# Kernel tuning notes

Hardware: AMD Instinct MI355X
Metric: run time of the kernel (lower is better)

The kernel has to match this reference:

```python
import jax, jax.numpy as jnp
import numpy as np

B, N_LINKS, N_JOINTS, C_L, C_J = 4096, 33, 32, 64, 128

def setup_inputs() -> dict:
    key = jax.random.key(0)
    k1, k2, k3, k4 = jax.random.split(key, 4)
    link_feats = jax.random.normal(k1, (B, N_LINKS, C_L, 16), dtype=jnp.float32)
    joint_feats = jax.random.normal(k2, (B, N_JOINTS, C_J), dtype=jnp.float32)
    # Stacked per-joint Linear weights: [J, C_L*16, C_J], bias [J, C_J]
    fan_in = C_L * 16
    W = jax.random.normal(k3, (N_JOINTS, fan_in, C_J), dtype=jnp.float32) / np.sqrt(fan_in).astype(np.float32)
    b = jax.random.normal(k4, (N_JOINTS, C_J), dtype=jnp.float32) * 0.01
    child_idx = jnp.arange(1, N_JOINTS + 1, dtype=jnp.int64)  # child link of joint j is link j+1
    return {"link_feats": link_feats, "joint_feats": joint_feats, "W": W, "b": b, "child_idx": child_idx}

def reference(link_feats, joint_feats, W, b, child_idx):
    # Gather child-link features per joint: [B, J, C_L, 16] -> flatten to [B, J, C_L*16]
    Bsz = link_feats.shape[0]
    J = child_idx.shape[0]
    x = link_feats[:, child_idx].reshape(Bsz, J, -1)
    # Grouped GEMM over joints (replaces Python loop of tiny Linears), + bias + residual
    return jnp.einsum('bji,jio->bjo', x, W) + b[None, :, :] + joint_feats
```

## Files before the change

### kernel.cpp

```cpp
#include <hip/hip_runtime.h>
#include <hip/hip_bf16.h>

typedef __attribute__((ext_vector_type(8))) short bf16x8;
typedef __attribute__((ext_vector_type(4))) float f32x4;

#define NB    4096
#define NLINK 33
#define NJ    32
#define KTOT  1024
#define CJ    128
#define BM    128
#define BK    64
#define NT    (KTOT / BK)

__device__ short g_Wf[NJ * KTOT * CJ];

static __device__ __forceinline__ short f2bf(float f) {
    unsigned u = __builtin_bit_cast(unsigned, f);
    unsigned r = u + 0x7FFFu + ((u >> 16) & 1u);
    return (short)(r >> 16);
}

__global__ __launch_bounds__(256) void conv_w(const float* __restrict__ W) {
    const int gid = blockIdx.x * 256 + threadIdx.x;
    const int q  = gid & 3;
    const int c  = (gid >> 2) & 127;
    const int kt = (gid >> 9) & 31;
    const int j  = gid >> 14;
    const float* src = W + ((size_t)j * KTOT + kt * 32 + q * 8) * CJ + c;
    bf16x8 v;
    #pragma unroll
    for (int e = 0; e < 8; ++e) v[e] = f2bf(src[(size_t)e * CJ]);
    reinterpret_cast<bf16x8*>(g_Wf)[gid] = v;
}

__global__ __launch_bounds__(512, 4) void joint_gemm(
    const float* __restrict__ link,
    const float* __restrict__ jf,
    const float* __restrict__ bias,
    const int*   __restrict__ child,
    float* __restrict__ out)
{
    __shared__ short lA[2][BM * BK];

    const int tid  = threadIdx.x;
    const int lane = tid & 63;
    const int wave = tid >> 6;
    const int wr   = wave >> 1;
    const int wc   = wave & 1;
    const int q    = lane >> 4;
    const int r    = lane & 15;
    const int xr   = r & 7;

    const int bx = blockIdx.x;
    const int j  = bx & 31;
    const int mt = bx >> 5;
    const int rowbase = mt * BM;
    const int cidx = child[j];

    const int srow   = tid >> 2;
    const int squart = tid & 3;
    const float* abase = link + ((size_t)(rowbase + srow) * NLINK + cidx) * KTOT + squart * 16;
    const int xw = srow & 7;
    const int p0 = (squart * 2) ^ xw;
    const int p1 = p0 ^ 1;

    const bf16x8* wb = reinterpret_cast<const bf16x8*>(g_Wf);
    const size_t bbase = ((size_t)j * 32 * 128 + wc * 64 + r) * 4 + q;

    f32x4  acc[2][4] = {};
    float4 fa4[4];
    bf16x8 Breg[2][4];

    auto loadA = [&](int t) {
        const float4* p = reinterpret_cast<const float4*>(abase + (size_t)t * BK);
        fa4[0] = p[0]; fa4[1] = p[1]; fa4[2] = p[2]; fa4[3] = p[3];
    };
    auto stageA = [&](int b) {
        const float* f = reinterpret_cast<const float*>(fa4);
        bf16x8 v0, v1;
        #pragma unroll
        for (int e = 0; e < 8; ++e) { v0[e] = f2bf(f[e]); v1[e] = f2bf(f[8 + e]); }
        bf16x8* Lw = reinterpret_cast<bf16x8*>(lA[b]) + srow * 8;
        Lw[p0] = v0;
        Lw[p1] = v1;
    };
    auto loadB = [&](int t) {
        #pragma unroll
        for (int kk = 0; kk < 2; ++kk)
            #pragma unroll
            for (int ni = 0; ni < 4; ++ni)
                Breg[kk][ni] = wb[bbase + (size_t)(t * 2 + kk) * 512 + ni * 64];
    };

    loadA(0);
    loadB(0);
    stageA(0);
    loadA(1);
    __syncthreads();

    int cur = 0;
    for (int t = 0; t < NT; ++t) {
        if (t + 1 < NT) stageA(cur ^ 1);
        if (t + 2 < NT) loadA(t + 2);

        const bf16x8* Lr = reinterpret_cast<const bf16x8*>(lA[cur]);
        #pragma unroll
        for (int kk = 0; kk < 2; ++kk) {
            bf16x8 af[2];
            #pragma unroll
            for (int mi = 0; mi < 2; ++mi) {
                const int R = wr * 32 + mi * 16 + r;
                af[mi] = Lr[R * 8 + (((kk << 2) | q) ^ xr)];
            }
            #pragma unroll
            for (int mi = 0; mi < 2; ++mi)
                #pragma unroll
                for (int ni = 0; ni < 4; ++ni)
                    acc[mi][ni] = __builtin_amdgcn_mfma_f32_16x16x32_bf16(
                        af[mi], Breg[kk][ni], acc[mi][ni], 0, 0, 0);
        }

        if (t + 1 < NT) loadB(t + 1);
        __syncthreads();
        cur ^= 1;
    }

    float bv[4];
    #pragma unroll
    for (int ni = 0; ni < 4; ++ni) bv[ni] = bias[j * CJ + wc * 64 + ni * 16 + r];

    #pragma unroll
    for (int mi = 0; mi < 2; ++mi) {
        #pragma unroll
        for (int rr = 0; rr < 4; ++rr) {
            const int bg = rowbase + wr * 32 + mi * 16 + q * 4 + rr;
            const size_t ob = ((size_t)bg * NJ + j) * CJ;
            #pragma unroll
            for (int ni = 0; ni < 4; ++ni) {
                const int o = wc * 64 + ni * 16 + r;
                out[ob + o] = acc[mi][ni][rr] + bv[ni] + jf[ob + o];
            }
        }
    }
}

extern "C" void kernel_launch(void* const* d_in, const int* in_sizes, int n_in,
                              void* d_out, int out_size, void* d_ws, size_t ws_size,
                              hipStream_t stream) {
    (void)in_sizes; (void)n_in; (void)out_size; (void)d_ws; (void)ws_size;
    const float* link  = (const float*)d_in[0];
    const float* jfeat = (const float*)d_in[1];
    const float* W     = (const float*)d_in[2];
    const float* bias  = (const float*)d_in[3];
    const int*   child = (const int*)d_in[4];
    float* out = (float*)d_out;

    conv_w<<<dim3((NJ * KTOT * CJ / 8) / 256), dim3(256), 0, stream>>>(W);
    joint_gemm<<<dim3(NJ * (NB / BM)), dim3(512), 0, stream>>>(link, jfeat, bias, child, out);
}
```

Baseline: 182.3 us.

## Drop LDS staging and feed MFMA A-fragments directly from registers

Removes the shared-memory A tile and its per-step __syncthreads. Each wave now loads its own 32 fp32 rows straight into registers in MFMA fragment layout and converts them to bf16 there. Each block shrinks to 4 waves, and each wave covers all 128 output columns, with a two-stage register double buffer for both A and B. The aim is to cut LDS traffic and barrier stalls in a memory-bound gather-GEMM. The cost is much higher register pressure (launch bounds of 256 threads, 2 blocks) and lower occupancy, which may leave too little memory latency hidden.

```diff
diff --git a/kernel.cpp b/kernel.cpp
--- a/kernel.cpp
+++ b/kernel.cpp
@@ -1,5 +1,4 @@
 #include <hip/hip_runtime.h>
-#include <hip/hip_bf16.h>
 
 typedef __attribute__((ext_vector_type(8))) short bf16x8;
 typedef __attribute__((ext_vector_type(4))) float f32x4;
@@ -9,9 +8,7 @@
 #define NJ    32
 #define KTOT  1024
 #define CJ    128
-#define BM    128
-#define BK    64
-#define NT    (KTOT / BK)
+#define NSTEP 32
 
 __device__ short g_Wf[NJ * KTOT * CJ];
 
@@ -34,111 +31,92 @@
     reinterpret_cast<bf16x8*>(g_Wf)[gid] = v;
 }
 
-__global__ __launch_bounds__(512, 4) void joint_gemm(
+__global__ __launch_bounds__(256, 2) void joint_gemm(
     const float* __restrict__ link,
     const float* __restrict__ jf,
     const float* __restrict__ bias,
     const int*   __restrict__ child,
     float* __restrict__ out)
 {
-    __shared__ short lA[2][BM * BK];
-
     const int tid  = threadIdx.x;
     const int lane = tid & 63;
     const int wave = tid >> 6;
-    const int wr   = wave >> 1;
-    const int wc   = wave & 1;
     const int q    = lane >> 4;
     const int r    = lane & 15;
-    const int xr   = r & 7;
 
     const int bx = blockIdx.x;
     const int j  = bx & 31;
     const int mt = bx >> 5;
-    const int rowbase = mt * BM;
+    const int row0 = mt * 128 + wave * 32;
     const int cidx = child[j];
 
-    const int srow   = tid >> 2;
-    const int squart = tid & 3;
-    const float* abase = link + ((size_t)(rowbase + srow) * NLINK + cidx) * KTOT + squart * 16;
-    const int xw = srow & 7;
-    const int p0 = (squart * 2) ^ xw;
-    const int p1 = p0 ^ 1;
+    const float* a0 = link + ((size_t)(row0 + r) * NLINK + cidx) * KTOT + q * 8;
+    const float* a1 = a0 + (size_t)16 * NLINK * KTOT;
 
     const bf16x8* wb = reinterpret_cast<const bf16x8*>(g_Wf);
-    const size_t bbase = ((size_t)j * 32 * 128 + wc * 64 + r) * 4 + q;
+    const size_t bb = ((size_t)j * 32 * 128 + r) * 4 + q;
 
-    f32x4  acc[2][4] = {};
-    float4 fa4[4];
-    bf16x8 Breg[2][4];
+    f32x4 acc[2][8] = {};
 
-    auto loadA = [&](int t) {
-        const float4* p = reinterpret_cast<const float4*>(abase + (size_t)t * BK);
-        fa4[0] = p[0]; fa4[1] = p[1]; fa4[2] = p[2]; fa4[3] = p[3];
+    float4 A0[4], A1[4];
+    bf16x8 B0[8], B1[8];
+
+    auto loadA = [&](float4* A, int t) {
+        const float4* p0 = reinterpret_cast<const float4*>(a0 + t * 32);
+        const float4* p1 = reinterpret_cast<const float4*>(a1 + t * 32);
+        A[0] = p0[0]; A[1] = p0[1]; A[2] = p1[0]; A[3] = p1[1];
     };
-    auto stageA = [&](int b) {
-        const float* f = reinterpret_cast<const float*>(fa4);
-        bf16x8 v0, v1;
+    auto loadB = [&](bf16x8* Bv, int t) {
+        const bf16x8* p = wb + bb + (size_t)t * 512;
         #pragma unroll
-        for (int e = 0; e < 8; ++e) { v0[e] = f2bf(f[e]); v1[e] = f2bf(f[8 + e]); }
-        bf16x8* Lw = reinterpret_cast<bf16x8*>(lA[b]) + srow * 8;
-        Lw[p0] = v0;
-        Lw[p1] = v1;
-    };
-    auto loadB = [&](int t) {
-        #pragma unroll
-        for (int kk = 0; kk < 2; ++kk)
-            #pragma unroll
-            for (int ni = 0; ni < 4; ++ni)
-                Breg[kk][ni] = wb[bbase + (size_t)(t * 2 + kk) * 512 + ni * 64];
+        for (int ni = 0; ni < 8; ++ni) Bv[ni] = p[ni * 64];
     };
 
-    loadA(0);
-    loadB(0);
-    stageA(0);
-    loadA(1);
-    __syncthreads();
+    loadA(A0, 0); loadB(B0, 0);
+    loadA(A1, 1); loadB(B1, 1);
 
-    int cur = 0;
-    for (int t = 0; t < NT; ++t) {
-        if (t + 1 < NT) stageA(cur ^ 1);
-        if (t + 2 < NT) loadA(t + 2);
-
-        const bf16x8* Lr = reinterpret_cast<const bf16x8*>(lA[cur]);
-        #pragma unroll
-        for (int kk = 0; kk < 2; ++kk) {
-            bf16x8 af[2];
+    for (int t = 0; t < NSTEP; t += 2) {
+        {
+            bf16x8 af0, af1;
+            const float* f = reinterpret_cast<const float*>(A0);
             #pragma unroll
-            for (int mi = 0; mi < 2; ++mi) {
-                const int R = wr * 32 + mi * 16 + r;
-                af[mi] = Lr[R * 8 + (((kk << 2) | q) ^ xr)];
+            for (int e = 0; e < 8; ++e) { af0[e] = f2bf(f[e]); af1[e] = f2bf(f[8 + e]); }
+            if (t + 2 < NSTEP) loadA(A0, t + 2);
+            #pragma unroll
+            for (int ni = 0; ni < 8; ++ni) {
+                acc[0][ni] = __builtin_amdgcn_mfma_f32_16x16x32_bf16(af0, B0[ni], acc[0][ni], 0, 0, 0);
+                acc[1][ni] = __builtin_amdgcn_mfma_f32_16x16x32_bf16(af1, B0[ni], acc[1][ni], 0, 0, 0);
             }
+            if (t + 2 < NSTEP) loadB(B0, t + 2);
+        }
+        {
+            bf16x8 af0, af1;
+            const float* f = reinterpret_cast<const float*>(A1);
             #pragma unroll
-            for (int mi = 0; mi < 2; ++mi)
-                #pragma unroll
-                for (int ni = 0; ni < 4; ++ni)
-                    acc[mi][ni] = __builtin_amdgcn_mfma_f32_16x16x32_bf16(
-                        af[mi], Breg[kk][ni], acc[mi][ni], 0, 0, 0);
+            for (int e = 0; e < 8; ++e) { af0[e] = f2bf(f[e]); af1[e] = f2bf(f[8 + e]); }
+            if (t + 3 < NSTEP) loadA(A1, t + 3);
+            #pragma unroll
+            for (int ni = 0; ni < 8; ++ni) {
+                acc[0][ni] = __builtin_amdgcn_mfma_f32_16x16x32_bf16(af0, B1[ni], acc[0][ni], 0, 0, 0);
+                acc[1][ni] = __builtin_amdgcn_mfma_f32_16x16x32_bf16(af1, B1[ni], acc[1][ni], 0, 0, 0);
+            }
+            if (t + 3 < NSTEP) loadB(B1, t + 3);
         }
-
-        if (t + 1 < NT) loadB(t + 1);
-        __syncthreads();
-        cur ^= 1;
     }
 
-    float bv[4];
+    float bv[8];
     #pragma unroll
-    for (int ni = 0; ni < 4; ++ni) bv[ni] = bias[j * CJ + wc * 64 + ni * 16 + r];
+    for (int ni = 0; ni < 8; ++ni) bv[ni] = bias[j * CJ + ni * 16 + r];
 
     #pragma unroll
     for (int mi = 0; mi < 2; ++mi) {
         #pragma unroll
         for (int rr = 0; rr < 4; ++rr) {
-            const int bg = rowbase + wr * 32 + mi * 16 + q * 4 + rr;
+            const int bg = row0 + mi * 16 + q * 4 + rr;
             const size_t ob = ((size_t)bg * NJ + j) * CJ;
             #pragma unroll
-            for (int ni = 0; ni < 4; ++ni) {
-                const int o = wc * 64 + ni * 16 + r;
+            for (int ni = 0; ni < 8; ++ni) {
+                const int o = ni * 16 + r;
                 out[ob + o] = acc[mi][ni][rr] + bv[ni] + jf[ob + o];
             }
         }
@@ -157,5 +135,5 @@
     float* out = (float*)d_out;
 
     conv_w<<<dim3((NJ * KTOT * CJ / 8) / 256), dim3(256), 0, stream>>>(W);
-    joint_gemm<<<dim3(NJ * (NB / BM)), dim3(512), 0, stream>>>(link, jfeat, bias, child, out);
+    joint_gemm<<<dim3(NJ * (NB / 128)), dim3(256), 0, stream>>>(link, jfeat, bias, child, out);
 }
```

After: 191.7 us. +5.1%, slower.
